# Kernel tuning notes

Hardware: AMD Instinct MI355X
Metric: run time of the kernel (lower is better)

The kernel has to match this reference:

```python
import jax, jax.numpy as jnp
import numpy as np

N_NODES = 50000
N_EDGES = 800000
DIM = 64
N_ETYPES = 4
N_STEPS = 5


def setup_inputs() -> dict:
    key = jax.random.key(0)
    ks = jax.random.split(key, 10)
    feat = jax.random.normal(ks[0], (N_NODES, DIM), dtype=jnp.float32)
    src = jax.random.randint(ks[1], (N_EDGES,), 0, N_NODES, dtype=jnp.int32)
    dst = jax.random.randint(ks[2], (N_EDGES,), 0, N_NODES, dtype=jnp.int32)
    etypes = jax.random.randint(ks[3], (N_EDGES,), 0, N_ETYPES, dtype=jnp.int32)
    # per-edge-type Linear weights, xavier_normal with relu gain, zero bias
    gain = float(np.sqrt(2.0))
    std = gain * float(np.sqrt(2.0 / (DIM + DIM)))
    W = jax.random.normal(ks[4], (N_ETYPES, DIM, DIM), dtype=jnp.float32) * std  # [T, out, in]
    b = jnp.zeros((N_ETYPES, DIM), dtype=jnp.float32)
    # GRUCell params (torch layout: [3*dim, dim], gates order r,z,n), uniform(-1/sqrt(dim), 1/sqrt(dim))
    bound = 1.0 / float(np.sqrt(DIM))
    w_ih = jax.random.uniform(ks[5], (3 * DIM, DIM), minval=-bound, maxval=bound, dtype=jnp.float32)
    w_hh = jax.random.uniform(ks[6], (3 * DIM, DIM), minval=-bound, maxval=bound, dtype=jnp.float32)
    b_ih = jax.random.uniform(ks[7], (3 * DIM,), minval=-bound, maxval=bound, dtype=jnp.float32)
    b_hh = jax.random.uniform(ks[8], (3 * DIM,), minval=-bound, maxval=bound, dtype=jnp.float32)
    return {"feat": feat, "W": W, "b": b, "w_ih": w_ih, "w_hh": w_hh,
            "b_ih": b_ih, "b_hh": b_hh, "src": src, "dst": dst, "etypes": etypes}


def _gru_cell(a, h, w_ih, w_hh, b_ih, b_hh):
    gi = a @ w_ih.T + b_ih  # [N, 3*D]
    gh = h @ w_hh.T + b_hh
    i_r, i_z, i_n = jnp.split(gi, 3, axis=-1)
    h_r, h_z, h_n = jnp.split(gh, 3, axis=-1)
    r = jax.nn.sigmoid(i_r + h_r)
    z = jax.nn.sigmoid(i_z + h_z)
    n = jnp.tanh(i_n + r * h_n)
    return (1.0 - z) * n + z * h


def reference(feat, W, b, w_ih, w_hh, b_ih, b_hh, src, dst, etypes):
    n_nodes = feat.shape[0]
    h = feat
    for _ in range(N_STEPS):
        # apply every etype linear to all nodes: [N, T, D]
        h_all = jnp.einsum('nd,ted->nte', h, W) + b
        # per-edge message selects src node under its edge type: [E, D]
        m = h_all[src, etypes]
        # scatter-sum to destination nodes: [N, D]
        a = jax.ops.segment_sum(m, dst, num_segments=n_nodes)
        h = _gru_cell(a, h, w_ih, w_hh, b_ih, b_hh)
    return h
```

## Files before the change

### kernel.cpp

```cpp
#include <hip/hip_runtime.h>
#include <hip/hip_bf16.h>
#include <cstdint>

#define DIM 64
#define TD 256
#define NSTEPS 5
#define HS  68
#define HHS 72
#define GLDH 194
#define MAXDEG 48

typedef __attribute__((ext_vector_type(8))) short short8v;
typedef __attribute__((ext_vector_type(4))) float f32x4;
typedef __attribute__((ext_vector_type(8))) _Float16 half8v;

__device__ __forceinline__ float fast_sigmoid(float x){
  return 1.0f / (1.0f + __expf(-x));
}
__device__ __forceinline__ float fast_tanh(float x){
  return 2.0f / (1.0f + __expf(-2.0f * x)) - 1.0f;
}

__device__ __forceinline__ unsigned short f2bf(float x){
  unsigned u = __builtin_bit_cast(unsigned, x);
  return (unsigned short)((u + 0x7FFFu + ((u>>16)&1u)) >> 16);
}
__device__ __forceinline__ float bf2f(unsigned short b){
  unsigned u = ((unsigned)b)<<16;
  return __builtin_bit_cast(float, u);
}

__device__ __forceinline__ void splitbf8(const float* __restrict__ p,
                                         short8v& hi, short8v& lo){
  float4 x0 = *(const float4*)p;
  float4 x1 = *(const float4*)(p+4);
  float xs[8] = {x0.x,x0.y,x0.z,x0.w,x1.x,x1.y,x1.z,x1.w};
#pragma unroll
  for(int i=0;i<8;i++){
    unsigned short hb = f2bf(xs[i]);
    float rem = xs[i] - bf2f(hb);
    hi[i] = (short)hb;
    lo[i] = (short)f2bf(rem);
  }
}

__global__ __launch_bounds__(256) void k_pack(const float* __restrict__ src,
    short* __restrict__ ph, short* __restrict__ pl, int ncoltiles){
  int idx = blockIdx.x*256 + threadIdx.x;
  int total = ncoltiles*1024;
  if (idx >= total) return;
  int e = idx & 7, lane = (idx>>3)&63, kc = (idx>>9)&1, ct = idx>>10;
  int col = ct*16 + (lane&15);
  int k = kc*32 + (lane>>4)*8 + e;
  float v = src[(size_t)col*64 + k];
  unsigned short hb = f2bf(v);
  ph[idx] = (short)hb;
  pl[idx] = (short)f2bf(v - bf2f(hb));
}

__global__ __launch_bounds__(256) void k_packh(const float* __restrict__ src,
    _Float16* __restrict__ ph, _Float16* __restrict__ pl, int ncoltiles, int mode){
  int idx = blockIdx.x*256 + threadIdx.x;
  int total = ncoltiles*1024;
  if (idx >= total) return;
  int e = idx & 7, lane = (idx>>3)&63, kc = (idx>>9)&1, ct = idx>>10;
  int col = ct*16 + (lane&15);
  int k = kc*32 + (lane>>4)*8 + e;
  float v;
  if (mode==0){ int t = col>>6, eo = col&63; v = src[(size_t)(t*64+eo)*64 + k]; }
  else        { v = src[(size_t)col*64 + k]; }
  _Float16 hv = (_Float16)v;
  ph[idx] = hv;
  pl[idx] = (_Float16)(v - (float)hv);
}

__global__ __launch_bounds__(256) void k_cast(const float* __restrict__ x,
                                              _Float16* __restrict__ y, int n4){
  int i = blockIdx.x*256 + threadIdx.x;
  if (i >= n4) return;
  float4 v = *(const float4*)(x + (size_t)i*4);
  y[(size_t)i*4+0] = (_Float16)v.x; y[(size_t)i*4+1] = (_Float16)v.y;
  y[(size_t)i*4+2] = (_Float16)v.z; y[(size_t)i*4+3] = (_Float16)v.w;
}

__global__ __launch_bounds__(256) void k_scatter_ell(
    const int* __restrict__ src, const int* __restrict__ dst,
    const int* __restrict__ et, int* __restrict__ deg,
    int* __restrict__ ell, int n_edges) {
  int e = blockIdx.x * 256 + threadIdx.x;
  if (e >= n_edges) return;
  int d0 = dst[e];
  int rank = atomicAdd(&deg[d0], 1);
  if (rank < MAXDEG)
    ell[(size_t)d0 * MAXDEG + rank] = (src[e] << 2) | et[e];
}

__global__ __launch_bounds__(256) void k_transform_mfma(
    const _Float16* __restrict__ hb, const _Float16* __restrict__ pth,
    const _Float16* __restrict__ ptl, const float* __restrict__ b,
    _Float16* __restrict__ h_all, int n_nodes){
  const int wave = threadIdx.x >> 6, lane = threadIdx.x & 63;
  const int n0 = blockIdx.x * 16;
  if (n0 >= n_nodes) return;
  const int arow = n0 + (lane & 15);
  const int kb = (lane >> 4) * 8;
  half8v ah0 = *(const half8v*)(hb + (size_t)arow*DIM + kb);
  half8v ah1 = *(const half8v*)(hb + (size_t)arow*DIM + 32 + kb);
  const int crow = n0 + (lane >> 4) * 4;
  const int cc = lane & 15;
#pragma unroll
  for (int i = 0; i < 4; ++i){
    int ct = wave*4 + i;
    const half8v bh0 = *(const half8v*)(pth + ((size_t)(ct*2+0)*64 + lane)*8);
    const half8v bh1 = *(const half8v*)(pth + ((size_t)(ct*2+1)*64 + lane)*8);
    const half8v bl0 = *(const half8v*)(ptl + ((size_t)(ct*2+0)*64 + lane)*8);
    const half8v bl1 = *(const half8v*)(ptl + ((size_t)(ct*2+1)*64 + lane)*8);
    float bias = b[ct*16 + cc];
    f32x4 acc = {bias,bias,bias,bias};
    acc = __builtin_amdgcn_mfma_f32_16x16x32_f16(ah0, bh0, acc, 0,0,0);
    acc = __builtin_amdgcn_mfma_f32_16x16x32_f16(ah1, bh1, acc, 0,0,0);
    acc = __builtin_amdgcn_mfma_f32_16x16x32_f16(ah0, bl0, acc, 0,0,0);
    acc = __builtin_amdgcn_mfma_f32_16x16x32_f16(ah1, bl1, acc, 0,0,0);
#pragma unroll
    for (int q=0;q<4;q++)
      h_all[(size_t)(crow + q)*TD + ct*16 + cc] = (_Float16)acc[q];
  }
}

__global__ __launch_bounds__(256) void k_step(
    const _Float16* __restrict__ h_in, _Float16* __restrict__ h_out,
    const int* __restrict__ ell, const int* __restrict__ deg,
    _Float16* __restrict__ hb, float* __restrict__ hfull,
    const short* __restrict__ pih_h, const short* __restrict__ pih_l,
    const _Float16* __restrict__ phh_h, const _Float16* __restrict__ phh_l,
    const float* __restrict__ b_ih, const float* __restrict__ b_hh,
    const _Float16* __restrict__ pth, const _Float16* __restrict__ ptl,
    const float* __restrict__ bb,
    int n_nodes, int do_transform, int write_out){
  __shared__ __align__(16) char smem[4352 + 12416];
  float    (*atile)[HS]  = (float(*)[HS])smem;
  _Float16 (*hnewh)[HHS] = (_Float16(*)[HHS])smem;
  _Float16* gbuf         = (_Float16*)(smem + 4352);

  const int tid = threadIdx.x;
  const int wave = tid >> 6, lane = tid & 63;
  const int n0 = blockIdx.x * 16;
  if (n0 >= n_nodes) return;

  {
    int j = tid >> 4;
    int q = tid & 15;
    int eslot = q >> 3;
    int dimg = q & 7;
    int node = n0 + j;
    int dg = min(deg[node], MAXDEG);
    const int* eb = ell + (size_t)node * MAXDEG;
    float acc[8] = {0,0,0,0,0,0,0,0};
    int i = eslot;
    for (; i + 6 < dg; i += 8) {
      int p0 = eb[i], p1 = eb[i+2], p2 = eb[i+4], p3 = eb[i+6];
      half8v v0 = *(const half8v*)(h_in + (size_t)(p0>>2)*TD + (p0&3)*DIM + dimg*8);
      half8v v1 = *(const half8v*)(h_in + (size_t)(p1>>2)*TD + (p1&3)*DIM + dimg*8);
      half8v v2 = *(const half8v*)(h_in + (size_t)(p2>>2)*TD + (p2&3)*DIM + dimg*8);
      half8v v3 = *(const half8v*)(h_in + (size_t)(p3>>2)*TD + (p3&3)*DIM + dimg*8);
#pragma unroll
      for (int k=0;k<8;k++)
        acc[k] += ((float)v0[k] + (float)v1[k]) + ((float)v2[k] + (float)v3[k]);
    }
    for (; i < dg; i += 2) {
      int p0 = eb[i];
      half8v v0 = *(const half8v*)(h_in + (size_t)(p0>>2)*TD + (p0&3)*DIM + dimg*8);
#pragma unroll
      for (int k=0;k<8;k++) acc[k] += (float)v0[k];
    }
#pragma unroll
    for (int k=0;k<8;k++) acc[k] += __shfl_xor(acc[k], 8);
    if (eslot == 0) {
#pragma unroll
      for (int k=0;k<8;k++) atile[j][dimg*8+k] = acc[k];
    }
  }
  __syncthreads();

  const int kb = (lane >> 4) * 8;
  const int rr = (lane >> 4) * 4;
  const int cc = lane & 15;

  if (wave < 2) {
    const float* xp = &atile[lane & 15][0];
    short8v ah0,al0,ah1,al1;
    splitbf8(xp + kb,      ah0, al0);
    splitbf8(xp + 32 + kb, ah1, al1);
    const int ct0 = (wave & 1) * 6;
#pragma unroll
    for (int i = 0; i < 6; ++i){
      int ct = ct0 + i;
      const short8v bh0 = *(const short8v*)(pih_h + ((size_t)(ct*2+0)*64 + lane)*8);
      const short8v bh1 = *(const short8v*)(pih_h + ((size_t)(ct*2+1)*64 + lane)*8);
      const short8v bl0 = *(const short8v*)(pih_l + ((size_t)(ct*2+0)*64 + lane)*8);
      const short8v bl1 = *(const short8v*)(pih_l + ((size_t)(ct*2+1)*64 + lane)*8);
      float bias = b_ih[ct*16 + cc];
      f32x4 acc = {bias,bias,bias,bias};
      acc = __builtin_amdgcn_mfma_f32_16x16x32_bf16(ah0, bh0, acc, 0,0,0);
      acc = __builtin_amdgcn_mfma_f32_16x16x32_bf16(ah1, bh1, acc, 0,0,0);
      acc = __builtin_amdgcn_mfma_f32_16x16x32_bf16(al0, bh0, acc, 0,0,0);
      acc = __builtin_amdgcn_mfma_f32_16x16x32_bf16(al1, bh1, acc, 0,0,0);
      acc = __builtin_amdgcn_mfma_f32_16x16x32_bf16(ah0, bl0, acc, 0,0,0);
      acc = __builtin_amdgcn_mfma_f32_16x16x32_bf16(ah1, bl1, acc, 0,0,0);
#pragma unroll
      for (int q=0;q<4;q++)
        gbuf[(rr+q)*GLDH + ct*16 + cc] = (_Float16)acc[q];
    }
  } else {
    _Float16* outb = gbuf + 16*GLDH;
    const _Float16* xp = hb + (size_t)(n0 + (lane & 15))*DIM;
    half8v ah0 = *(const half8v*)(xp + kb);
    half8v ah1 = *(const half8v*)(xp + 32 + kb);
    const int ct0 = (wave & 1) * 6;
#pragma unroll
    for (int i = 0; i < 6; ++i){
      int ct = ct0 + i;
      const half8v bh0 = *(const half8v*)(phh_h + ((size_t)(ct*2+0)*64 + lane)*8);
      const half8v bh1 = *(const half8v*)(phh_h + ((size_t)(ct*2+1)*64 + lane)*8);
      const half8v bl0 = *(const half8v*)(phh_l + ((size_t)(ct*2+0)*64 + lane)*8);
      const half8v bl1 = *(const half8v*)(phh_l + ((size_t)(ct*2+1)*64 + lane)*8);
      float bias = b_hh[ct*16 + cc];
      f32x4 acc = {bias,bias,bias,bias};
      acc = __builtin_amdgcn_mfma_f32_16x16x32_f16(ah0, bh0, acc, 0,0,0);
      acc = __builtin_amdgcn_mfma_f32_16x16x32_f16(ah1, bh1, acc, 0,0,0);
      acc = __builtin_amdgcn_mfma_f32_16x16x32_f16(ah0, bl0, acc, 0,0,0);
      acc = __builtin_amdgcn_mfma_f32_16x16x32_f16(ah1, bl1, acc, 0,0,0);
#pragma unroll
      for (int q=0;q<4;q++)
        outb[(rr+q)*GLDH + ct*16 + cc] = (_Float16)acc[q];
    }
  }
  __syncthreads();

#pragma unroll
  for (int it=0; it<4; ++it){
    int t = it*256 + tid;
    int j = t >> 6, d = t & 63;
    float gir = (float)gbuf[j*GLDH + d];
    float giz = (float)gbuf[j*GLDH + 64 + d];
    float gin = (float)gbuf[j*GLDH + 128 + d];
    float ghr = (float)gbuf[16*GLDH + j*GLDH + d];
    float ghz = (float)gbuf[16*GLDH + j*GLDH + 64 + d];
    float ghn = (float)gbuf[16*GLDH + j*GLDH + 128 + d];
    float r  = fast_sigmoid(gir + ghr);
    float z  = fast_sigmoid(giz + ghz);
    float nv = fast_tanh   (gin + r*ghn);
    size_t off = (size_t)(n0+j)*DIM + d;
    float ho = (float)hb[off];
    float hn = (1.0f - z)*nv + z*ho;
    _Float16 hq = (_Float16)hn;
    hb[off] = hq;
    if (write_out) hfull[off] = hn;
    hnewh[j][d] = hq;
  }
  if (!do_transform) return;
  __syncthreads();

  half8v th0 = *(const half8v*)(&hnewh[lane & 15][kb]);
  half8v th1 = *(const half8v*)(&hnewh[lane & 15][32 + kb]);
  const int crow = n0 + (lane >> 4) * 4;
#pragma unroll
  for (int i = 0; i < 4; ++i){
    int ct = wave*4 + i;
    const half8v bh0 = *(const half8v*)(pth + ((size_t)(ct*2+0)*64 + lane)*8);
    const half8v bh1 = *(const half8v*)(pth + ((size_t)(ct*2+1)*64 + lane)*8);
    const half8v bl0 = *(const half8v*)(ptl + ((size_t)(ct*2+0)*64 + lane)*8);
    const half8v bl1 = *(const half8v*)(ptl + ((size_t)(ct*2+1)*64 + lane)*8);
    float bias = bb[ct*16 + cc];
    f32x4 acc = {bias,bias,bias,bias};
    acc = __builtin_amdgcn_mfma_f32_16x16x32_f16(th0, bh0, acc, 0,0,0);
    acc = __builtin_amdgcn_mfma_f32_16x16x32_f16(th1, bh1, acc, 0,0,0);
    acc = __builtin_amdgcn_mfma_f32_16x16x32_f16(th0, bl0, acc, 0,0,0);
    acc = __builtin_amdgcn_mfma_f32_16x16x32_f16(th1, bl1, acc, 0,0,0);
#pragma unroll
    for (int q=0;q<4;q++)
      h_out[(size_t)(crow + q)*TD + ct*16 + cc] = (_Float16)acc[q];
  }
}

extern "C" void kernel_launch(void* const* d_in, const int* in_sizes, int n_in,
                              void* d_out, int out_size, void* d_ws, size_t ws_size,
                              hipStream_t stream) {
  const float* feat = (const float*)d_in[0];
  const float* W    = (const float*)d_in[1];
  const float* b    = (const float*)d_in[2];
  const float* w_ih = (const float*)d_in[3];
  const float* w_hh = (const float*)d_in[4];
  const float* b_ih = (const float*)d_in[5];
  const float* b_hh = (const float*)d_in[6];
  const int* src = (const int*)d_in[7];
  const int* dst = (const int*)d_in[8];
  const int* et  = (const int*)d_in[9];

  const int n_nodes = in_sizes[0] / DIM;
  const int n_edges = in_sizes[7];

  float* hfull = (float*)d_out;
  char* ws = (char*)d_ws;
  _Float16* hall0 = (_Float16*)ws;  ws += (size_t)n_nodes * TD * sizeof(_Float16);
  _Float16* hall1 = (_Float16*)ws;  ws += (size_t)n_nodes * TD * sizeof(_Float16);
  _Float16* hb    = (_Float16*)ws;  ws += (size_t)n_nodes * DIM * sizeof(_Float16);
  int* ell     = (int*)ws;      ws += (size_t)n_nodes * MAXDEG * sizeof(int);
  int* deg     = (int*)ws;      ws += (size_t)n_nodes * sizeof(int);
  _Float16* pt_h  = (_Float16*)ws;  ws += 16384 * sizeof(_Float16);
  _Float16* pt_l  = (_Float16*)ws;  ws += 16384 * sizeof(_Float16);
  short* pih_h = (short*)ws;    ws += 12288 * sizeof(short);
  short* pih_l = (short*)ws;    ws += 12288 * sizeof(short);
  _Float16* phh_h = (_Float16*)ws;  ws += 12288 * sizeof(_Float16);
  _Float16* phh_l = (_Float16*)ws;  ws += 12288 * sizeof(_Float16);

  k_packh<<<64, 256, 0, stream>>>(W,    pt_h,  pt_l,  16, 0);
  k_pack <<<48, 256, 0, stream>>>(w_ih, pih_h, pih_l, 12);
  k_packh<<<48, 256, 0, stream>>>(w_hh, phh_h, phh_l, 12, 1);
  k_cast<<<(n_nodes*DIM/4 + 255)/256, 256, 0, stream>>>(feat, hb, n_nodes*DIM/4);

  const int nblk_edges = (n_edges + 255) / 256;
  hipMemsetAsync(deg, 0, (size_t)n_nodes * sizeof(int), stream);
  k_scatter_ell<<<nblk_edges, 256, 0, stream>>>(src, dst, et, deg, ell, n_edges);

  const int rtiles = (n_nodes + 15) / 16;

  k_transform_mfma<<<rtiles, 256, 0, stream>>>(hb, pt_h, pt_l, b, hall0, n_nodes);
  for (int s = 0; s < NSTEPS; ++s) {
    const _Float16* hin = (s & 1) ? hall1 : hall0;
    _Float16* hout      = (s & 1) ? hall0 : hall1;
    k_step<<<rtiles, 256, 0, stream>>>(hin, hout, ell, deg, hb, hfull,
                                       pih_h, pih_l, phh_h, phh_l, b_ih, b_hh,
                                       pt_h, pt_l, b, n_nodes,
                                       (s < NSTEPS - 1) ? 1 : 0,
                                       (s == NSTEPS - 1) ? 1 : 0);
  }
}
```

Baseline: 297.4 us.

## Merge weight pack kernels, deepen gather unroll, skip final-step half stores

The three weight-packing launches are folded into one kernel that dispatches on block index, saving two launches. The neighbour-gather loop now handles 16 edges per iteration (8 loads in flight per thread) to expose more memory-level parallelism. On the last step, the fp16 state and shared-memory writes are skipped and only the fp32 output is written. More unrolling raises register pressure, which could lower occupancy.

After: 301.3 us. No clear change (+1.3%).

```diff
diff --git a/kernel.cpp b/kernel.cpp
--- a/kernel.cpp
+++ b/kernel.cpp
@@ -44,34 +44,42 @@
   }
 }
 
-__global__ __launch_bounds__(256) void k_pack(const float* __restrict__ src,
-    short* __restrict__ ph, short* __restrict__ pl, int ncoltiles){
-  int idx = blockIdx.x*256 + threadIdx.x;
-  int total = ncoltiles*1024;
-  if (idx >= total) return;
-  int e = idx & 7, lane = (idx>>3)&63, kc = (idx>>9)&1, ct = idx>>10;
-  int col = ct*16 + (lane&15);
-  int k = kc*32 + (lane>>4)*8 + e;
-  float v = src[(size_t)col*64 + k];
-  unsigned short hb = f2bf(v);
-  ph[idx] = (short)hb;
-  pl[idx] = (short)f2bf(v - bf2f(hb));
-}
-
-__global__ __launch_bounds__(256) void k_packh(const float* __restrict__ src,
-    _Float16* __restrict__ ph, _Float16* __restrict__ pl, int ncoltiles, int mode){
-  int idx = blockIdx.x*256 + threadIdx.x;
-  int total = ncoltiles*1024;
-  if (idx >= total) return;
-  int e = idx & 7, lane = (idx>>3)&63, kc = (idx>>9)&1, ct = idx>>10;
-  int col = ct*16 + (lane&15);
-  int k = kc*32 + (lane>>4)*8 + e;
-  float v;
-  if (mode==0){ int t = col>>6, eo = col&63; v = src[(size_t)(t*64+eo)*64 + k]; }
-  else        { v = src[(size_t)col*64 + k]; }
-  _Float16 hv = (_Float16)v;
-  ph[idx] = hv;
-  pl[idx] = (_Float16)(v - (float)hv);
+__global__ __launch_bounds__(256) void k_pack_all(
+    const float* __restrict__ W, const float* __restrict__ w_ih,
+    const float* __restrict__ w_hh,
+    _Float16* __restrict__ pt_h, _Float16* __restrict__ pt_l,
+    short* __restrict__ pih_h, short* __restrict__ pih_l,
+    _Float16* __restrict__ phh_h, _Float16* __restrict__ phh_l){
+  int blk = blockIdx.x;
+  if (blk < 64) {
+    int idx = blk*256 + threadIdx.x;
+    int e = idx & 7, lane = (idx>>3)&63, kc = (idx>>9)&1, ct = idx>>10;
+    int col = ct*16 + (lane&15);
+    int k = kc*32 + (lane>>4)*8 + e;
+    int t = col>>6, eo = col&63;
+    float v = W[(size_t)(t*64+eo)*64 + k];
+    _Float16 hv = (_Float16)v;
+    pt_h[idx] = hv;
+    pt_l[idx] = (_Float16)(v - (float)hv);
+  } else if (blk < 112) {
+    int idx = (blk-64)*256 + threadIdx.x;
+    int e = idx & 7, lane = (idx>>3)&63, kc = (idx>>9)&1, ct = idx>>10;
+    int col = ct*16 + (lane&15);
+    int k = kc*32 + (lane>>4)*8 + e;
+    float v = w_ih[(size_t)col*64 + k];
+    unsigned short hb = f2bf(v);
+    pih_h[idx] = (short)hb;
+    pih_l[idx] = (short)f2bf(v - bf2f(hb));
+  } else {
+    int idx = (blk-112)*256 + threadIdx.x;
+    int e = idx & 7, lane = (idx>>3)&63, kc = (idx>>9)&1, ct = idx>>10;
+    int col = ct*16 + (lane&15);
+    int k = kc*32 + (lane>>4)*8 + e;
+    float v = w_hh[(size_t)col*64 + k];
+    _Float16 hv = (_Float16)v;
+    phh_h[idx] = hv;
+    phh_l[idx] = (_Float16)(v - (float)hv);
+  }
 }
 
 __global__ __launch_bounds__(256) void k_cast(const float* __restrict__ x,
@@ -157,7 +165,21 @@
     const int* eb = ell + (size_t)node * MAXDEG;
     float acc[8] = {0,0,0,0,0,0,0,0};
     int i = eslot;
-    for (; i + 6 < dg; i += 8) {
+    while (i + 14 < dg) {
+      int p[8];
+#pragma unroll
+      for (int k2=0;k2<8;k2++) p[k2] = eb[i + 2*k2];
+      half8v v[8];
+#pragma unroll
+      for (int k2=0;k2<8;k2++)
+        v[k2] = *(const half8v*)(h_in + (size_t)(p[k2]>>2)*TD + (p[k2]&3)*DIM + dimg*8);
+#pragma unroll
+      for (int k2=0;k2<8;k2++)
+#pragma unroll
+        for (int k=0;k<8;k++) acc[k] += (float)v[k2][k];
+      i += 16;
+    }
+    if (i + 6 < dg) {
       int p0 = eb[i], p1 = eb[i+2], p2 = eb[i+4], p3 = eb[i+6];
       half8v v0 = *(const half8v*)(h_in + (size_t)(p0>>2)*TD + (p0&3)*DIM + dimg*8);
       half8v v1 = *(const half8v*)(h_in + (size_t)(p1>>2)*TD + (p1&3)*DIM + dimg*8);
@@ -166,6 +188,7 @@
 #pragma unroll
       for (int k=0;k<8;k++)
         acc[k] += ((float)v0[k] + (float)v1[k]) + ((float)v2[k] + (float)v3[k]);
+      i += 8;
     }
     for (; i < dg; i += 2) {
       int p0 = eb[i];
@@ -253,10 +276,13 @@
     size_t off = (size_t)(n0+j)*DIM + d;
     float ho = (float)hb[off];
     float hn = (1.0f - z)*nv + z*ho;
-    _Float16 hq = (_Float16)hn;
-    hb[off] = hq;
-    if (write_out) hfull[off] = hn;
-    hnewh[j][d] = hq;
+    if (write_out) {
+      hfull[off] = hn;
+    } else {
+      _Float16 hq = (_Float16)hn;
+      hb[off] = hq;
+      hnewh[j][d] = hq;
+    }
   }
   if (!do_transform) return;
   __syncthreads();
@@ -314,9 +340,8 @@
   _Float16* phh_h = (_Float16*)ws;  ws += 12288 * sizeof(_Float16);
   _Float16* phh_l = (_Float16*)ws;  ws += 12288 * sizeof(_Float16);
 
-  k_packh<<<64, 256, 0, stream>>>(W,    pt_h,  pt_l,  16, 0);
-  k_pack <<<48, 256, 0, stream>>>(w_ih, pih_h, pih_l, 12);
-  k_packh<<<48, 256, 0, stream>>>(w_hh, phh_h, phh_l, 12, 1);
+  k_pack_all<<<160, 256, 0, stream>>>(W, w_ih, w_hh, pt_h, pt_l,
+                                      pih_h, pih_l, phh_h, phh_l);
   k_cast<<<(n_nodes*DIM/4 + 255)/256, 256, 0, stream>>>(feat, hb, n_nodes*DIM/4);
 
   const int nblk_edges = (n_edges + 255) / 256;
```
